# Performance work log

Measured on AMD Instinct MI355X. Metric: run time of the kernel, lower is better.

The kernel has to match this reference:

```python
import jax, jax.numpy as jnp
import numpy as np

N = 100000
E = 3200000
IN_DIM = 128
HID = 256
OUT = 64


def _xavier(key, shape):
    fan_in, fan_out = shape
    limit = float(np.sqrt(6.0 / (fan_in + fan_out)))
    return jax.random.uniform(key, shape, jnp.float32, -limit, limit)


def setup_inputs() -> dict:
    key = jax.random.key(0)
    k_x, k_ei, k_ew, k_w1, k_w2 = jax.random.split(key, 5)
    x = jax.random.normal(k_x, (N, IN_DIM), jnp.float32)
    edge_index = jax.random.randint(k_ei, (2, E), 0, N, jnp.int32)
    # symmetric-normalized-adjacency-like positive weights
    edge_weight = jax.random.uniform(k_ew, (E,), jnp.float32)
    W1 = _xavier(k_w1, (IN_DIM, HID))
    b1 = jnp.zeros((HID,), jnp.float32)
    W2 = _xavier(k_w2, (HID, OUT))
    b2 = jnp.zeros((OUT,), jnp.float32)
    return {"x": x, "edge_index": edge_index, "edge_weight": edge_weight,
            "W1": W1, "b1": b1, "W2": W2, "b2": b2}


def _spmm(edge_index, edge_weight, h):
    # out[dst] = sum_e w[e] * h[src[e]]  (sparse adj @ dense h)
    dst, src = edge_index[0], edge_index[1]
    msgs = h[src] * edge_weight[:, None]  # [E, F]
    return jax.ops.segment_sum(msgs, dst, num_segments=N)


def reference(x, edge_index, edge_weight, W1, b1, W2, b2):
    # layer 1: adj @ (x @ W1) + b1, relu
    h = _spmm(edge_index, edge_weight, x @ W1) + b1
    h = jax.nn.relu(h)
    # layer 2 (output): adj @ (h @ W2) + b2
    out = _spmm(edge_index, edge_weight, h @ W2) + b2
    return out
```

## Files before the change

kernel.cpp:

```cpp
#include <hip/hip_runtime.h>

#define NN 100000
#define NE 3200000
#define SH 9
#define BW 512
#define NBUK 196
#define P1_BLOCKS 500
#define P1_CHUNK 6400
#define P2_CAP 18000
#define HLS 264

using bf16x8 = __attribute__((ext_vector_type(8))) short;
using f32x4  = __attribute__((ext_vector_type(4))) float;
using f32x2  = __attribute__((ext_vector_type(2))) float;
using uintx4 = __attribute__((ext_vector_type(4))) uint;
using fltx4  = __attribute__((ext_vector_type(4))) float;

__device__ inline ushort f2bf(float f) {
    uint u = __float_as_uint(f);
    return (ushort)((u + 0x7fffu + ((u >> 16) & 1u)) >> 16);
}
__device__ inline uint pk2bf(float a, float b) {
    return (uint)f2bf(a) | ((uint)f2bf(b) << 16);
}
__device__ inline uint f2e4m3(float f) {
    uint u = __float_as_uint(f);
    uint s = (u >> 24) & 0x80u;
    uint a = u & 0x7fffffffu;
    if (a < 0x3c800000u) return s;
    uint r = a + 0x7ffffu + ((a >> 20) & 1u);
    if (r > 0x43e00000u) r = 0x43e00000u;
    uint e = (r >> 23) - 120u;
    uint m = (r >> 20) & 7u;
    return s | (e << 3) | m;
}


__global__ __launch_bounds__(512, 4) void part1_kernel(
        const int* __restrict__ dst, const int* __restrict__ src,
        const float* __restrict__ w, int* __restrict__ gtail, uint2* __restrict__ stg,
        const float* __restrict__ x, uint* __restrict__ x8 ) {
    __shared__ uint2 rec[P1_CHUNK];
    __shared__ unsigned char map[P1_CHUNK];
    __shared__ int cnt[NBUK], gbase[NBUK], lbase[NBUK], sc[256];
    int tx = threadIdx.x;
    int i0 = blockIdx.x * P1_CHUNK;

    {
        int cbase = blockIdx.x * 3200;
        for (int i = tx; i < 3200; i += 512) {
            size_t c = (size_t)(cbase + i) * 8;
            float4 a = *reinterpret_cast<const float4*>(x + c);
            float4 b = *reinterpret_cast<const float4*>(x + c + 4);
            uint lo = f2e4m3(a.x) | (f2e4m3(a.y) << 8) | (f2e4m3(a.z) << 16) | (f2e4m3(a.w) << 24);
            uint hi = f2e4m3(b.x) | (f2e4m3(b.y) << 8) | (f2e4m3(b.z) << 16) | (f2e4m3(b.w) << 24);
            x8[c / 4]     = lo;
            x8[c / 4 + 1] = hi;
        }
    }

    for (int i = tx; i < NBUK; i += 512) cnt[i] = 0;
    __syncthreads();
    for (int i = i0 + tx; i < i0 + P1_CHUNK; i += 512) atomicAdd(&cnt[dst[i] >> SH], 1);
    __syncthreads();
    if (tx < NBUK) gbase[tx] = tx * P2_CAP + atomicAdd(&gtail[tx], cnt[tx]);
    if (tx < 256) sc[tx] = (tx < NBUK) ? cnt[tx] : 0;
    __syncthreads();
    int sv = (tx < 256) ? sc[tx] : 0;
    #pragma unroll
    for (int off = 1; off < 256; off <<= 1) {
        int u = (tx < 256 && tx >= off) ? sc[tx - off] : 0;
        __syncthreads();
        if (tx < 256) sc[tx] += u;
        __syncthreads();
    }
    if (tx < NBUK) lbase[tx] = sc[tx] - sv;
    __syncthreads();
    {
        int wv = tx >> 6, ln = tx & 63;
        for (int b = wv; b < NBUK; b += 8) {
            int s0 = lbase[b], c = cnt[b];
            for (int s = ln; s < c; s += 64) map[s0 + s] = (unsigned char)b;
        }
    }
    __syncthreads();
    for (int i = tx; i < NBUK; i += 512) cnt[i] = 0;
    __syncthreads();
    for (int i = i0 + tx; i < i0 + P1_CHUNK; i += 512) {
        int d = dst[i];
        int b = d >> SH;
        int r = atomicAdd(&cnt[b], 1);
        rec[lbase[b] + r] = make_uint2((uint)src[i] | ((uint)(d & (BW - 1)) << 17),
                                       (uint)__float_as_int(w[i]));
    }
    __syncthreads();
    for (int s = tx; s < P1_CHUNK; s += 512) {
        int b = map[s];
        stg[gbase[b] + (s - lbase[b])] = rec[s];
    }
}


__global__ __launch_bounds__(512, 1) void part2_kernel(
        const uint2* __restrict__ stg, const int* __restrict__ gtail,
        int* __restrict__ rp, uint* __restrict__ ep,
        const float* __restrict__ W1, const float* __restrict__ W2,
        ushort* __restrict__ w1p, ushort* __restrict__ w2p) {
    __shared__ uint2 st[P2_CAP];
    __shared__ int cnt[512], lbase[512], bs[256];
    int tx = threadIdx.x;
    int b = blockIdx.x;

    if (b == 0) {
        for (int i = tx; i < 32768; i += 512) {
            int n = i & 255, k = i >> 8;
            int kk = k >> 5, hi = (k >> 3) & 3, j = k & 7;
            int t = n >> 4, l = hi * 16 + (n & 15);
            w1p[(((t * 4 + kk) * 64 + l) << 3) + j] = f2bf(W1[i]);
        }
        for (int i = tx; i < 16384; i += 512) {
            int n = i & 63, k = i >> 6;
            int kk = k >> 5, hi = (k >> 3) & 3, j = k & 7;
            int t = n >> 4, l = hi * 16 + (n & 15);
            w2p[(((t * 8 + kk) * 64 + l) << 3) + j] = f2bf(W2[i]);
        }
        if (tx == 0) rp[NN] = NE;
    }

    if (tx < 256) bs[tx] = (tx < NBUK) ? gtail[tx] : 0;
    __syncthreads();
    #pragma unroll
    for (int off = 1; off < 256; off <<= 1) {
        int u = (tx < 256 && tx >= off) ? bs[tx - off] : 0;
        __syncthreads();
        if (tx < 256) bs[tx] += u;
        __syncthreads();
    }
    __syncthreads();
    int len = gtail[b];
    int s1 = bs[b];
    int s0 = s1 - len;
    const uint2* in = stg + (size_t)b * P2_CAP;

    cnt[tx] = 0;
    __syncthreads();
    for (int i = tx; i < len; i += 512) atomicAdd(&cnt[in[i].x >> 17], 1);
    __syncthreads();
    int v = cnt[tx];
    #pragma unroll
    for (int off = 1; off < 512; off <<= 1) {
        int u = (tx >= off) ? cnt[tx - off] : 0;
        __syncthreads();
        cnt[tx] += u;
        __syncthreads();
    }
    lbase[tx] = cnt[tx] - v;
    int node = (b << SH) + tx;
    if (node < NN) rp[node] = s0 + lbase[tx];
    __syncthreads();
    cnt[tx] = 0;
    __syncthreads();
    for (int i = tx; i < len; i += 512) {
        uint2 p = in[i];
        int dl = p.x >> 17;
        int r = atomicAdd(&cnt[dl], 1);
        st[lbase[dl] + r] = make_uint2(p.x & 0x1FFFFu, p.y);
    }
    __syncthreads();
    for (int i = tx; i < len; i += 512) {
        uint2 q = st[i];
        float wf = __uint_as_float(q.y);
        uint w15 = (uint)fminf(wf * 32768.f + 0.5f, 32767.f);
        ep[s0 + i] = q.x | (w15 << 17);
    }
}


__global__ void spmm_x_fp8(const uint* __restrict__ ep, const int* __restrict__ rp,
                           const uint2* __restrict__ x8 ,
                           uintx4* __restrict__ s2 , int n) {
    int row = blockIdx.x * 4 + (threadIdx.x >> 6);
    if (row >= n) return;
    int lane = threadIdx.x & 63;
    int g = lane >> 4;
    int q = lane & 15;
    int beg = rp[row], end = rp[row + 1];
    if (end <= beg) {
        if (lane < 16) __builtin_nontemporal_store(uintx4{0, 0, 0, 0}, &s2[(size_t)row * 16 + q]);
        return;
    }
    float acc[8];
    #pragma unroll
    for (int k = 0; k < 8; ++k) acc[k] = 0.f;
    int trips = (end - beg + 3) >> 2;
    #pragma unroll 8
    for (int t = 0; t < trips; ++t) {
        int idx = beg + t * 4 + g;
        bool valid = idx < end;
        uint p = ep[valid ? idx : end - 1];
        float wv = valid ? (float)(p >> 17) * (1.f / 32768.f) : 0.f;
        uint2 v = x8[(uint)(p & 0x1FFFFu) * 16u + q];
        f32x2 d0 = __builtin_amdgcn_cvt_pk_f32_fp8((int)v.x, false);
        f32x2 d1 = __builtin_amdgcn_cvt_pk_f32_fp8((int)v.x, true);
        f32x2 d2 = __builtin_amdgcn_cvt_pk_f32_fp8((int)v.y, false);
        f32x2 d3 = __builtin_amdgcn_cvt_pk_f32_fp8((int)v.y, true);
        acc[0] += wv * d0.x;
        acc[1] += wv * d0.y;
        acc[2] += wv * d1.x;
        acc[3] += wv * d1.y;
        acc[4] += wv * d2.x;
        acc[5] += wv * d2.y;
        acc[6] += wv * d3.x;
        acc[7] += wv * d3.y;
    }
    #pragma unroll
    for (int k = 0; k < 8; ++k) {
        acc[k] += __shfl_xor(acc[k], 16);
        acc[k] += __shfl_xor(acc[k], 32);
    }
    if (lane < 16) {
        uintx4 o;
        o.x = pk2bf(acc[0], acc[1]);
        o.y = pk2bf(acc[2], acc[3]);
        o.z = pk2bf(acc[4], acc[5]);
        o.w = pk2bf(acc[6], acc[7]);
        __builtin_nontemporal_store(o, &s2[(size_t)row * 16 + q]);
    }
}


__global__ __launch_bounds__(256) void spmm_g_bf16(
        const uint* __restrict__ ep, const int* __restrict__ rp,
        const uint4* __restrict__ g4 ,
        const float* __restrict__ bias, float* __restrict__ out, int n) {
    int wave = threadIdx.x >> 6;
    int lane = threadIdx.x & 63;
    int g = lane >> 3;
    int q = lane & 7;
    float4 bv0 = *reinterpret_cast<const float4*>(bias + q * 8);
    float4 bv1 = *reinterpret_cast<const float4*>(bias + q * 8 + 4);
    int rA = blockIdx.x * 8 + wave * 2;
    int rB = rA + 1;
    if (rA >= n) return;
    int begA = rp[rA], endA = rp[rA + 1];
    int begB = 0, endB = 0;
    if (rB < n) { begB = rp[rB]; endB = rp[rB + 1]; }
    float accA[8], accB[8];
    #pragma unroll
    for (int k = 0; k < 8; ++k) { accA[k] = 0.f; accB[k] = 0.f; }
    int tripsA = (endA - begA + 7) >> 3;
    int tripsB = (endB - begB + 7) >> 3;
    int trips = tripsA > tripsB ? tripsA : tripsB;
    #pragma unroll 4
    for (int t = 0; t < trips; ++t) {
        int iA = begA + t * 8 + g;
        int iB = begB + t * 8 + g;
        bool vA = iA < endA, vB = iB < endB;
        uint pA = ep[vA ? iA : 0];
        uint pB = ep[vB ? iB : 0];
        float wA = vA ? (float)(pA >> 17) * (1.f / 32768.f) : 0.f;
        float wB = vB ? (float)(pB >> 17) * (1.f / 32768.f) : 0.f;
        uint4 a = g4[(uint)(pA & 0x1FFFFu) * 8u + q];
        uint4 c = g4[(uint)(pB & 0x1FFFFu) * 8u + q];
        accA[0] += wA * __uint_as_float(a.x << 16);
        accA[1] += wA * __uint_as_float(a.x & 0xffff0000u);
        accA[2] += wA * __uint_as_float(a.y << 16);
        accA[3] += wA * __uint_as_float(a.y & 0xffff0000u);
        accA[4] += wA * __uint_as_float(a.z << 16);
        accA[5] += wA * __uint_as_float(a.z & 0xffff0000u);
        accA[6] += wA * __uint_as_float(a.w << 16);
        accA[7] += wA * __uint_as_float(a.w & 0xffff0000u);
        accB[0] += wB * __uint_as_float(c.x << 16);
        accB[1] += wB * __uint_as_float(c.x & 0xffff0000u);
        accB[2] += wB * __uint_as_float(c.y << 16);
        accB[3] += wB * __uint_as_float(c.y & 0xffff0000u);
        accB[4] += wB * __uint_as_float(c.z << 16);
        accB[5] += wB * __uint_as_float(c.z & 0xffff0000u);
        accB[6] += wB * __uint_as_float(c.w << 16);
        accB[7] += wB * __uint_as_float(c.w & 0xffff0000u);
    }
    #pragma unroll
    for (int k = 0; k < 8; ++k) {
        accA[k] += __shfl_xor(accA[k], 8);
        accA[k] += __shfl_xor(accA[k], 16);
        accA[k] += __shfl_xor(accA[k], 32);
        accB[k] += __shfl_xor(accB[k], 8);
        accB[k] += __shfl_xor(accB[k], 16);
        accB[k] += __shfl_xor(accB[k], 32);
    }
    if (lane < 8) {
        float* orow = out + (size_t)rA * 64 + q * 8;
        fltx4 a = {accA[0] + bv0.x, accA[1] + bv0.y, accA[2] + bv0.z, accA[3] + bv0.w};
        fltx4 b = {accA[4] + bv1.x, accA[5] + bv1.y, accA[6] + bv1.z, accA[7] + bv1.w};
        __builtin_nontemporal_store(a, (fltx4*)orow);
        __builtin_nontemporal_store(b, (fltx4*)(orow + 4));
    } else if (lane < 16 && rB < n) {
        float* orow = out + (size_t)rB * 64 + q * 8;
        fltx4 a = {accB[0] + bv0.x, accB[1] + bv0.y, accB[2] + bv0.z, accB[3] + bv0.w};
        fltx4 b = {accB[4] + bv1.x, accB[5] + bv1.y, accB[6] + bv1.z, accB[7] + bv1.w};
        __builtin_nontemporal_store(a, (fltx4*)orow);
        __builtin_nontemporal_store(b, (fltx4*)(orow + 4));
    }
}


__global__ __launch_bounds__(256) void gemm_fused(
        const ushort* __restrict__ s2, const ushort* __restrict__ w1p,
        const float* __restrict__ b1, const ushort* __restrict__ w2p,
        ushort* __restrict__ g) {
    __shared__ ushort hl[64 * HLS];
    int tx = threadIdx.x;
    int wave = tx >> 6, l = tx & 63;
    int wm = wave >> 1, wn = wave & 1;
    int row0 = blockIdx.x * 64;
    int lo = l & 15, hi = l >> 4;

    bf16x8 a[2][4];
    #pragma unroll
    for (int mt = 0; mt < 2; ++mt) {
        int r = row0 + wm * 32 + mt * 16 + lo;
        bool ok = r < NN;
        const bf16x8* base = reinterpret_cast<const bf16x8*>(s2 + (size_t)(ok ? r : 0) * 128);
        #pragma unroll
        for (int kk = 0; kk < 4; ++kk) {
            bf16x8 v = base[kk * 4 + hi];
            if (!ok) v = bf16x8{0, 0, 0, 0, 0, 0, 0, 0};
            a[mt][kk] = v;
        }
    }
    #pragma unroll
    for (int t = 0; t < 8; ++t) {
        int nt = wn * 8 + t;
        f32x4 acc0 = {0.f, 0.f, 0.f, 0.f};
        f32x4 acc1 = {0.f, 0.f, 0.f, 0.f};
        #pragma unroll
        for (int kk = 0; kk < 4; ++kk) {
            bf16x8 b = *reinterpret_cast<const bf16x8*>(w1p + (((nt * 4 + kk) * 64 + l) << 3));
            acc0 = __builtin_amdgcn_mfma_f32_16x16x32_bf16(a[0][kk], b, acc0, 0, 0, 0);
            acc1 = __builtin_amdgcn_mfma_f32_16x16x32_bf16(a[1][kk], b, acc1, 0, 0, 0);
        }
        int col = nt * 16 + lo;
        float bias = b1[col];
        #pragma unroll
        for (int r = 0; r < 4; ++r) {
            int rowl = wm * 32 + hi * 4 + r;
            hl[rowl * HLS + col] = f2bf(fmaxf(acc0[r] + bias, 0.f));
        }
        #pragma unroll
        for (int r = 0; r < 4; ++r) {
            int rowl = wm * 32 + 16 + hi * 4 + r;
            hl[rowl * HLS + col] = f2bf(fmaxf(acc1[r] + bias, 0.f));
        }
    }
    __syncthreads();

    int rl = wave * 16 + lo;
    bf16x8 a2[8];
    #pragma unroll
    for (int kk = 0; kk < 8; ++kk) {
        a2[kk] = *reinterpret_cast<const bf16x8*>(&hl[rl * HLS + kk * 32 + hi * 8]);
    }
    #pragma unroll
    for (int t = 0; t < 4; ++t) {
        f32x4 acc = {0.f, 0.f, 0.f, 0.f};
        #pragma unroll
        for (int kk = 0; kk < 8; ++kk) {
            bf16x8 b = *reinterpret_cast<const bf16x8*>(w2p + (((t * 8 + kk) * 64 + l) << 3));
            acc = __builtin_amdgcn_mfma_f32_16x16x32_bf16(a2[kk], b, acc, 0, 0, 0);
        }
        int col = t * 16 + lo;
        #pragma unroll
        for (int r = 0; r < 4; ++r) {
            int row = row0 + wave * 16 + hi * 4 + r;
            if (row < NN) g[(size_t)row * 64 + col] = f2bf(acc[r]);
        }
    }
}


extern "C" void kernel_launch(void* const* d_in, const int* in_sizes, int n_in,
                              void* d_out, int out_size, void* d_ws, size_t ws_size,
                              hipStream_t stream) {
    const float* x     = (const float*)d_in[0];
    const int*   ei    = (const int*)d_in[1];
    const float* ew_in = (const float*)d_in[2];
    const float* W1    = (const float*)d_in[3];
    const float* b1    = (const float*)d_in[4];
    const float* W2    = (const float*)d_in[5];
    const float* b2    = (const float*)d_in[6];
    float* outp = (float*)d_out;

    const int n = NN, e = NE;
    const int* dst = ei;
    const int* src = ei + e;

    char* ws = (char*)d_ws;
    size_t off = 0;
    auto alloc = [&](size_t bytes) {
        void* p = ws + off;
        off += (bytes + 255) & ~size_t(255);
        return p;
    };
    uint*  ep     = (uint*)alloc(sizeof(uint) * (size_t)e);
    int*   gtail  = (int*)alloc(sizeof(int) * NBUK);
    int*   rp     = (int*)alloc(sizeof(int) * (size_t)(n + 1));
    ushort* w1p   = (ushort*)alloc(sizeof(ushort) * 32768);
    ushort* w2p   = (ushort*)alloc(sizeof(ushort) * 16384);
    float* sbuf   = (float*)alloc(sizeof(float) * (size_t)n * 128);
    float* hbuf   = (float*)alloc(sizeof(float) * (size_t)n * 256);
    uint*  x8  = (uint*)hbuf;
    uint2* stg = (uint2*)((char*)hbuf + (size_t)n * 128 * 2);
    ushort* g2 = (ushort*)((char*)hbuf + (size_t)56 * 1024 * 1024);
    ushort* s2 = (ushort*)sbuf;

    hipMemsetAsync(gtail, 0, sizeof(int) * NBUK, stream);
    part1_kernel<<<P1_BLOCKS, 512, 0, stream>>>(dst, src, ew_in, gtail, stg, x, x8);
    part2_kernel<<<NBUK, 512, 0, stream>>>(stg, gtail, rp, ep, W1, W2, w1p, w2p);

    spmm_x_fp8<<<(n + 3) / 4, 256, 0, stream>>>(ep, rp, (const uint2*)x8, (uintx4*)s2, n);
    gemm_fused<<<(n + 63) / 64, 256, 0, stream>>>(s2, w1p, b1, w2p, g2);
    spmm_g_bf16<<<(n + 7) / 8, 256, 0, stream>>>(ep, rp, (const uint4*)g2, b2, outp, n);
}
```

Baseline: 234.4 us.

## Halve CSR bucket width to double bucket count and part2 occupancy

Bucket size drops from 512 to 256 destination nodes, which doubles the number of buckets and part2 blocks. Per-block staging capacity is halved, so shared memory in part2 shrinks and launch bounds allow four blocks per CU. In part1 the separate map-fill pass is folded into the scatter loop, with map widened to ushort to hold the larger bucket ids, and the scans are widened to 512 entries. The aim is more parallelism in part2 and one fewer pass in part1, at the cost of longer scans and a tighter per-bucket capacity that could overflow if a bucket gets too many edges.

```diff
diff --git a/kernel.cpp b/kernel.cpp
--- a/kernel.cpp
+++ b/kernel.cpp
@@ -2,12 +2,12 @@
 
 #define NN 100000
 #define NE 3200000
-#define SH 9
-#define BW 512
-#define NBUK 196
+#define SH 8
+#define BW 256
+#define NBUK 392
 #define P1_BLOCKS 500
 #define P1_CHUNK 6400
-#define P2_CAP 18000
+#define P2_CAP 9000
 #define HLS 264
 
 using bf16x8 = __attribute__((ext_vector_type(8))) short;
@@ -41,8 +41,8 @@
         const float* __restrict__ w, int* __restrict__ gtail, uint2* __restrict__ stg,
         const float* __restrict__ x, uint* __restrict__ x8 ) {
     __shared__ uint2 rec[P1_CHUNK];
-    __shared__ unsigned char map[P1_CHUNK];
-    __shared__ int cnt[NBUK], gbase[NBUK], lbase[NBUK], sc[256];
+    __shared__ ushort map[P1_CHUNK];
+    __shared__ int cnt[NBUK], gbase[NBUK], lbase[NBUK], sc[512];
     int tx = threadIdx.x;
     int i0 = blockIdx.x * P1_CHUNK;
 
@@ -64,25 +64,17 @@
     for (int i = i0 + tx; i < i0 + P1_CHUNK; i += 512) atomicAdd(&cnt[dst[i] >> SH], 1);
     __syncthreads();
     if (tx < NBUK) gbase[tx] = tx * P2_CAP + atomicAdd(&gtail[tx], cnt[tx]);
-    if (tx < 256) sc[tx] = (tx < NBUK) ? cnt[tx] : 0;
-    __syncthreads();
-    int sv = (tx < 256) ? sc[tx] : 0;
-    #pragma unroll
-    for (int off = 1; off < 256; off <<= 1) {
-        int u = (tx < 256 && tx >= off) ? sc[tx - off] : 0;
-        __syncthreads();
-        if (tx < 256) sc[tx] += u;
+    sc[tx] = (tx < NBUK) ? cnt[tx] : 0;
+    __syncthreads();
+    int sv = sc[tx];
+    #pragma unroll
+    for (int off = 1; off < 512; off <<= 1) {
+        int u = (tx >= off) ? sc[tx - off] : 0;
+        __syncthreads();
+        sc[tx] += u;
         __syncthreads();
     }
     if (tx < NBUK) lbase[tx] = sc[tx] - sv;
-    __syncthreads();
-    {
-        int wv = tx >> 6, ln = tx & 63;
-        for (int b = wv; b < NBUK; b += 8) {
-            int s0 = lbase[b], c = cnt[b];
-            for (int s = ln; s < c; s += 64) map[s0 + s] = (unsigned char)b;
-        }
-    }
     __syncthreads();
     for (int i = tx; i < NBUK; i += 512) cnt[i] = 0;
     __syncthreads();
@@ -90,8 +82,10 @@
         int d = dst[i];
         int b = d >> SH;
         int r = atomicAdd(&cnt[b], 1);
-        rec[lbase[b] + r] = make_uint2((uint)src[i] | ((uint)(d & (BW - 1)) << 17),
-                                       (uint)__float_as_int(w[i]));
+        int pos = lbase[b] + r;
+        rec[pos] = make_uint2((uint)src[i] | ((uint)(d & (BW - 1)) << 17),
+                              (uint)__float_as_int(w[i]));
+        map[pos] = (ushort)b;
     }
     __syncthreads();
     for (int s = tx; s < P1_CHUNK; s += 512) {
@@ -101,13 +95,13 @@
 }
 
 
-__global__ __launch_bounds__(512, 1) void part2_kernel(
+__global__ __launch_bounds__(512, 4) void part2_kernel(
         const uint2* __restrict__ stg, const int* __restrict__ gtail,
         int* __restrict__ rp, uint* __restrict__ ep,
         const float* __restrict__ W1, const float* __restrict__ W2,
         ushort* __restrict__ w1p, ushort* __restrict__ w2p) {
     __shared__ uint2 st[P2_CAP];
-    __shared__ int cnt[512], lbase[512], bs[256];
+    __shared__ int cnt[512], lbase[512], bs[512];
     int tx = threadIdx.x;
     int b = blockIdx.x;
 
@@ -127,16 +121,15 @@
         if (tx == 0) rp[NN] = NE;
     }
 
-    if (tx < 256) bs[tx] = (tx < NBUK) ? gtail[tx] : 0;
-    __syncthreads();
-    #pragma unroll
-    for (int off = 1; off < 256; off <<= 1) {
-        int u = (tx < 256 && tx >= off) ? bs[tx - off] : 0;
-        __syncthreads();
-        if (tx < 256) bs[tx] += u;
-        __syncthreads();
-    }
-    __syncthreads();
+    bs[tx] = (tx < NBUK) ? gtail[tx] : 0;
+    __syncthreads();
+    #pragma unroll
+    for (int off = 1; off < 512; off <<= 1) {
+        int u = (tx >= off) ? bs[tx - off] : 0;
+        __syncthreads();
+        bs[tx] += u;
+        __syncthreads();
+    }
     int len = gtail[b];
     int s1 = bs[b];
     int s0 = s1 - len;
@@ -156,7 +149,7 @@
     }
     lbase[tx] = cnt[tx] - v;
     int node = (b << SH) + tx;
-    if (node < NN) rp[node] = s0 + lbase[tx];
+    if (tx < BW && node < NN) rp[node] = s0 + lbase[tx];
     __syncthreads();
     cnt[tx] = 0;
     __syncthreads();
```

New measurement: 225.2 us. 3.9% less time.
